# Kernel optimization log

Hardware: AMD Instinct MI355X
Metric: run time of the kernel (lower is better)

## Reference

```python
import jax, jax.numpy as jnp
import numpy as np

S, B, E, H = 2048, 2, 1024, 16
HD = E // H


def setup_inputs() -> dict:
    key = jax.random.key(0)
    ks = jax.random.split(key, 8)
    sc = 0.05
    return {
        "query": jax.random.normal(ks[0], (S, B, E), jnp.float32),
        "key": jax.random.normal(ks[1], (S, B, E), jnp.float32),
        "value": jax.random.normal(ks[2], (S, B, E), jnp.float32),
        "position_bias": jax.random.normal(ks[3], (B, S, S), jnp.float32) * sc,
        "in_proj_weight": jax.random.normal(ks[4], (3 * E, E), jnp.float32) * sc,
        "in_proj_bias": jnp.zeros((3 * E,), jnp.float32),
        "out_w": jax.random.normal(ks[5], (E, E), jnp.float32) * sc,
        "out_b": jnp.zeros((E,), jnp.float32),
    }


def reference(query, key, value, position_bias, in_proj_weight, in_proj_bias, out_w, out_b):
    # packed in-projection: w is (3E, E) in q,k,v order
    w_q, w_k, w_v = jnp.split(in_proj_weight, 3, axis=0)
    b_q, b_k, b_v = jnp.split(in_proj_bias, 3, axis=0)
    q = query @ w_q.T + b_q          # (S, B, E)
    k = key @ w_k.T + b_k
    v = value @ w_v.T + b_v
    # split heads: (S, B, H, HD)
    q = q.reshape(S, B, H, HD)
    k = k.reshape(S, B, H, HD)
    v = v.reshape(S, B, H, HD)
    scale = 1.0 / jnp.sqrt(jnp.float32(HD))
    # scores: (B, H, tgt, src)
    scores = jnp.einsum("qbhd,kbhd->bhqk", q * scale, k)
    scores = scores + position_bias[:, None, :, :]
    attn = jax.nn.softmax(scores, axis=-1)
    out = jnp.einsum("bhqk,kbhd->qbhd", attn, v).reshape(S, B, E)
    out = out @ out_w.T + out_b      # (S, B, E)
    attn_weights = attn.reshape(B * H, S, S)
    return out, attn_weights
```

## Files before the change

### kernel.cpp

```cpp
#include <hip/hip_runtime.h>

#define S_ 2048
#define B_ 2
#define E_ 1024
#define H_ 16

typedef _Float16 f16x8 __attribute__((ext_vector_type(8)));
typedef _Float16 f16x4 __attribute__((ext_vector_type(4)));
typedef _Float16 f16x2 __attribute__((ext_vector_type(2)));
typedef float f32x4 __attribute__((ext_vector_type(4)));
typedef unsigned short us4_t __attribute__((ext_vector_type(4)));
typedef unsigned u32x4 __attribute__((ext_vector_type(4)));
typedef unsigned u32x2 __attribute__((ext_vector_type(2)));

static __device__ __forceinline__ unsigned short f2h(float x) {
  _Float16 h = (_Float16)x;
  return __builtin_bit_cast(unsigned short, h);
}
static __device__ __forceinline__ unsigned pk_f16(float a, float b) {
  auto r = __builtin_amdgcn_cvt_pkrtz(a, b);
  return __builtin_bit_cast(unsigned, r);
}

__global__ void k_cvt_all(const float* __restrict__ q, const float* __restrict__ k,
                          const float* __restrict__ v, const float* __restrict__ ipw,
                          const float* __restrict__ outw, const float* __restrict__ posb,
                          unsigned short* __restrict__ qx, unsigned short* __restrict__ kx,
                          unsigned short* __restrict__ vx, unsigned short* __restrict__ w3,
                          unsigned short* __restrict__ ow, unsigned short* __restrict__ pb16) {
  const int M1 = 1 << 20;
  int i = blockIdx.x * blockDim.x + threadIdx.x;
  int stp = gridDim.x * blockDim.x;
  for (; i < 6 * M1; i += stp) {
    const float* src;
    unsigned short* dst;
    int j;
    if (i < M1)                   { src = q;    dst = qx;   j = i; }
    else if (i < 2 * M1)          { src = k;    dst = kx;   j = i - M1; }
    else if (i < 3 * M1)          { src = v;    dst = vx;   j = i - 2 * M1; }
    else if (i < 3 * M1 + 786432) { src = ipw;  dst = w3;   j = i - 3 * M1; }
    else if (i < 4 * M1)          { src = outw; dst = ow;   j = i - 3 * M1 - 786432; }
    else                          { src = posb; dst = pb16; j = i - 4 * M1; }
    f32x4 x = ((const f32x4*)src)[j];
    us4_t h;
    #pragma unroll
    for (int e = 0; e < 4; ++e) h[e] = f2h(x[e]);
    ((us4_t*)dst)[j] = h;
  }
}

__launch_bounds__(256, 2)
__global__ void k_proj_qk(const unsigned short* __restrict__ qx, const unsigned short* __restrict__ kx,
                          const unsigned short* __restrict__ wqk, const float* __restrict__ bias,
                          unsigned short* __restrict__ qf, unsigned short* __restrict__ kf) {
  const int z = blockIdx.z;
  const unsigned short* A = z ? kx : qx;
  const unsigned short* W = wqk + (size_t)z * (1024 * 1024);
  unsigned short* C = z ? kf : qf;
  const float* bia = bias + z * 1024;
  const float scale = z ? 1.0f : 0.125f;

  __shared__ unsigned short sA[128][40], sB[128][40];

  const int t = threadIdx.x;
  const int wid = t >> 6, l = t & 63, g = l >> 4, c = l & 15;
  const int wr = wid >> 1, wc = wid & 1;
  const int mb = blockIdx.x * 128, nb = blockIdx.y * 128;
  const int sr = t >> 1, sc = (t & 1) * 16;

  f32x4 acc[4][4] = {};

  for (int k0 = 0; k0 < 1024; k0 += 32) {
    __syncthreads();
    {
      const unsigned short* pa = A + (size_t)(mb + sr) * 1024 + k0 + sc;
      const unsigned short* pb = W + (size_t)(nb + sr) * 1024 + k0 + sc;
      *(f16x8*)&sA[sr][sc]     = *(const f16x8*)pa;
      *(f16x8*)&sA[sr][sc + 8] = *(const f16x8*)(pa + 8);
      *(f16x8*)&sB[sr][sc]     = *(const f16x8*)pb;
      *(f16x8*)&sB[sr][sc + 8] = *(const f16x8*)(pb + 8);
    }
    __syncthreads();
    f16x8 af[4], bf[4];
    #pragma unroll
    for (int i = 0; i < 4; ++i) {
      af[i] = *(const f16x8*)&sA[wr * 64 + i * 16 + c][g * 8];
      bf[i] = *(const f16x8*)&sB[wc * 64 + i * 16 + c][g * 8];
    }
    #pragma unroll
    for (int i = 0; i < 4; ++i)
      #pragma unroll
      for (int j = 0; j < 4; ++j)
        acc[i][j] = __builtin_amdgcn_mfma_f32_16x16x32_f16(af[i], bf[j], acc[i][j], 0, 0, 0);
  }
  #pragma unroll
  for (int i = 0; i < 4; ++i)
    #pragma unroll
    for (int j = 0; j < 4; ++j)
      #pragma unroll
      for (int rr = 0; rr < 4; ++rr) {
        int m = mb + wr * 64 + i * 16 + 4 * g + rr;
        int n = nb + wc * 64 + j * 16 + c;
        float v = (acc[i][j][rr] + bia[n]) * scale;
        C[(size_t)m * 1024 + n] = f2h(v);
      }
}

__launch_bounds__(256, 2)
__global__ void k_proj_v(const unsigned short* __restrict__ wv, const unsigned short* __restrict__ vx,
                         const float* __restrict__ bias, unsigned short* __restrict__ VT) {
  __shared__ unsigned short sA[128][40], sB[128][40];
  const int t = threadIdx.x;
  const int wid = t >> 6, l = t & 63, g = l >> 4, c = l & 15;
  const int wr = wid >> 1, wc = wid & 1;
  const int mb = blockIdx.x * 128;
  const int nb = blockIdx.y * 128;
  const int bb = nb >> 11;
  const int jb = nb & 2047;
  const int sr = t >> 1, sc = (t & 1) * 16;

  f32x4 acc[4][4] = {};
  for (int k0 = 0; k0 < 1024; k0 += 32) {
    __syncthreads();
    {
      const unsigned short* pa = wv + (size_t)(mb + sr) * 1024 + k0 + sc;
      const unsigned short* pb = vx + ((size_t)(jb + sr) * 2 + bb) * 1024 + k0 + sc;
      *(f16x8*)&sA[sr][sc]     = *(const f16x8*)pa;
      *(f16x8*)&sA[sr][sc + 8] = *(const f16x8*)(pa + 8);
      *(f16x8*)&sB[sr][sc]     = *(const f16x8*)pb;
      *(f16x8*)&sB[sr][sc + 8] = *(const f16x8*)(pb + 8);
    }
    __syncthreads();
    f16x8 af[4], bf[4];
    #pragma unroll
    for (int i = 0; i < 4; ++i) {
      af[i] = *(const f16x8*)&sA[wr * 64 + i * 16 + c][g * 8];
      bf[i] = *(const f16x8*)&sB[wc * 64 + i * 16 + c][g * 8];
    }
    #pragma unroll
    for (int i = 0; i < 4; ++i)
      #pragma unroll
      for (int j = 0; j < 4; ++j)
        acc[i][j] = __builtin_amdgcn_mfma_f32_16x16x32_f16(af[i], bf[j], acc[i][j], 0, 0, 0);
  }
  #pragma unroll
  for (int i = 0; i < 4; ++i)
    #pragma unroll
    for (int j = 0; j < 4; ++j)
      #pragma unroll
      for (int rr = 0; rr < 4; ++rr) {
        int m = mb + wr * 64 + i * 16 + 4 * g + rr;
        int jj = jb + wc * 64 + j * 16 + c;
        float v = acc[i][j][rr] + bias[2048 + m];
        VT[(size_t)bb * (1024 * 2048) + (size_t)m * 2048 + jj] = f2h(v);
      }
}

__launch_bounds__(256, 4)
__global__ void k_attn_pv(const unsigned short* __restrict__ qf, const unsigned short* __restrict__ kf,
                          const unsigned short* __restrict__ VT, const unsigned short* __restrict__ pb16,
                          float* __restrict__ attn, unsigned short* __restrict__ oc) {
  const int swz = (int)((blockIdx.x & 7) * 512 + (blockIdx.x >> 3));
  const int h = swz >> 8;
  const int b = (swz >> 7) & 1;
  const int qt = swz & 127;

  const int t = threadIdx.x;
  const int wid = t >> 6, l = t & 63, g = l >> 4, c = l & 15;
  const int ct = wid;

  __shared__ unsigned smem[8192];
  __shared__ float lds_red[4][16];
  unsigned* S_k = smem;
  unsigned* S_v = smem + 4096;

  const size_t qoff = ((size_t)(qt * 16 + c) * 2 + b) * 1024 + h * 64 + g * 8;
  const f16x8 qfr0 = *(const f16x8*)(qf + qoff);
  const f16x8 qfr1 = *(const f16x8*)(qf + qoff + 32);

  const unsigned short* kfb = kf + (size_t)b * 1024 + h * 64;
  const unsigned short* vtb = VT + ((size_t)b * 1024 + h * 64) * 2048;
  const unsigned short* pbRow = pb16 + (size_t)b * S_ * S_ + (size_t)(qt * 16 + c) * S_ + ct * 16;

  const int rb = t >> 3;
  const int lsl = (t & 7) ^ (rb & 7);

  #define LDSRD(base, row, slot) \
    __builtin_bit_cast(f16x8, *(const u32x4*)&(base)[(row) * 32 + ((((slot) ^ ((row) & 7))) * 4)])

  #define GLDS(stg, buf) do { \
    __builtin_amdgcn_global_load_lds( \
        (const __attribute__((address_space(1))) unsigned*)(kfb + (size_t)((stg) * 64 + rb) * 2048 + lsl * 8), \
        (__attribute__((address_space(3))) unsigned*)&S_k[(buf) * 2048 + wid * 256], 16, 0, 0); \
    __builtin_amdgcn_global_load_lds( \
        (const __attribute__((address_space(1))) unsigned*)(kfb + (size_t)((stg) * 64 + rb + 32) * 2048 + lsl * 8), \
        (__attribute__((address_space(3))) unsigned*)&S_k[(buf) * 2048 + 1024 + wid * 256], 16, 0, 0); \
    __builtin_amdgcn_global_load_lds( \
        (const __attribute__((address_space(1))) unsigned*)(vtb + (size_t)rb * 2048 + (stg) * 64 + lsl * 8), \
        (__attribute__((address_space(3))) unsigned*)&S_v[(buf) * 2048 + wid * 256], 16, 0, 0); \
    __builtin_amdgcn_global_load_lds( \
        (const __attribute__((address_space(1))) unsigned*)(vtb + (size_t)(rb + 32) * 2048 + (stg) * 64 + lsl * 8), \
        (__attribute__((address_space(3))) unsigned*)&S_v[(buf) * 2048 + 1024 + wid * 256], 16, 0, 0); \
  } while (0)

  f32x4 bias[2];
  unsigned psc0[32], psc1[32];
  float lsum = 0.f;
  f32x4 oacc[4] = {};

  GLDS(0, 0);
  {
    f16x4 b0 = *(const f16x4*)(pbRow + 4 * g);
    bias[0][0] = (float)b0[0] - 8.f; bias[0][1] = (float)b0[1] - 8.f;
    bias[0][2] = (float)b0[2] - 8.f; bias[0][3] = (float)b0[3] - 8.f;
  }
  __syncthreads();

  #pragma unroll
  for (int st = 0; st < 32; ++st) {
    const int cur = st & 1;
    if (st < 31) GLDS(st + 1, cur ^ 1);
    if (st < 31) {
      f16x4 bb = *(const f16x4*)(pbRow + (st + 1) * 64 + 4 * g);
      bias[cur ^ 1][0] = (float)bb[0] - 8.f; bias[cur ^ 1][1] = (float)bb[1] - 8.f;
      bias[cur ^ 1][2] = (float)bb[2] - 8.f; bias[cur ^ 1][3] = (float)bb[3] - 8.f;
    }

    {
      const int row = ct * 16 + c;
      const unsigned* kb = S_k + cur * 2048;
      f16x8 kfr0 = LDSRD(kb, row, g);
      f16x8 kfr1 = LDSRD(kb, row, 4 + g);
      f32x4 aA = {}, aB = {};
      aA = __builtin_amdgcn_mfma_f32_16x16x32_f16(kfr0, qfr0, aA, 0, 0, 0);
      aB = __builtin_amdgcn_mfma_f32_16x16x32_f16(kfr1, qfr1, aB, 0, 0, 0);
      float p0 = __expf(aA[0] + aB[0] + bias[cur][0]);
      float p1 = __expf(aA[1] + aB[1] + bias[cur][1]);
      float p2 = __expf(aA[2] + aB[2] + bias[cur][2]);
      float p3 = __expf(aA[3] + aB[3] + bias[cur][3]);
      lsum += (p0 + p1) + (p2 + p3);
      psc0[st] = pk_f16(p0, p1);
      psc1[st] = pk_f16(p2, p3);
    }

    {
      u32x2 br; br[0] = psc0[st]; br[1] = psc1[st];
      const f16x4 bfrag = __builtin_bit_cast(f16x4, br);
      const unsigned* vb = S_v + cur * 2048;
      #pragma unroll
      for (int dt = 0; dt < 4; ++dt) {
        const int row = dt * 16 + c;
        const int sl = (2 * ct + (g >> 1)) ^ (row & 7);
        u32x2 ar = *(const u32x2*)&vb[row * 32 + sl * 4 + 2 * (g & 1)];
        oacc[dt] = __builtin_amdgcn_mfma_f32_16x16x16f16(__builtin_bit_cast(f16x4, ar), bfrag, oacc[dt], 0, 0, 0);
      }
    }

    __syncthreads();
  }

  lsum += __shfl_xor(lsum, 16, 64);
  lsum += __shfl_xor(lsum, 32, 64);
  if (l < 16) lds_red[wid][l] = lsum;
  __syncthreads();
  const float inv = 1.0f / ((lds_red[0][c] + lds_red[1][c]) + (lds_red[2][c] + lds_red[3][c]));

  float* ored = (float*)smem;
  #pragma unroll
  for (int dt = 0; dt < 4; ++dt) {
    f32x4 o = oacc[dt];
    o[0] *= inv; o[1] *= inv; o[2] *= inv; o[3] *= inv;
    *(f32x4*)&ored[(wid * 16 + c) * 68 + dt * 16 + 4 * g] = o;
  }
  __syncthreads();
  {
    const int q = t >> 4;
    const int d0 = (t & 15) * 4;
    f32x4 s0 = *(const f32x4*)&ored[(0 * 16 + q) * 68 + d0];
    f32x4 s1 = *(const f32x4*)&ored[(1 * 16 + q) * 68 + d0];
    f32x4 s2 = *(const f32x4*)&ored[(2 * 16 + q) * 68 + d0];
    f32x4 s3 = *(const f32x4*)&ored[(3 * 16 + q) * 68 + d0];
    f32x4 s;
    s[0] = (s0[0] + s1[0]) + (s2[0] + s3[0]);
    s[1] = (s0[1] + s1[1]) + (s2[1] + s3[1]);
    s[2] = (s0[2] + s1[2]) + (s2[2] + s3[2]);
    s[3] = (s0[3] + s1[3]) + (s2[3] + s3[3]);
    u32x2 pk;
    pk[0] = pk_f16(s[0], s[1]);
    pk[1] = pk_f16(s[2], s[3]);
    *(u32x2*)&oc[((size_t)(qt * 16 + q) * 2 + b) * 1024 + h * 64 + d0] = pk;
  }

  float* arow = attn + ((size_t)(b * 16 + h) * S_ + qt * 16 + c) * S_ + ct * 16;
  #pragma unroll
  for (int st = 0; st < 32; ++st) {
    f16x2 h0 = __builtin_bit_cast(f16x2, psc0[st]);
    f16x2 h1 = __builtin_bit_cast(f16x2, psc1[st]);
    f32x4 o;
    o[0] = (float)h0[0] * inv;
    o[1] = (float)h0[1] * inv;
    o[2] = (float)h1[0] * inv;
    o[3] = (float)h1[1] * inv;
    *(f32x4*)(arow + (size_t)st * 64 + 4 * g) = o;
  }
  #undef LDSRD
  #undef GLDS
}

__launch_bounds__(256, 2)
__global__ void k_outproj(const unsigned short* __restrict__ oc, const unsigned short* __restrict__ ow,
                          const float* __restrict__ ob, float* __restrict__ out) {
  __shared__ unsigned short sA[128][40], sB[128][40];
  const int t = threadIdx.x;
  const int wid = t >> 6, l = t & 63, g = l >> 4, c = l & 15;
  const int wr = wid >> 1, wc = wid & 1;
  const int mb = blockIdx.x * 128, nb = blockIdx.y * 128;
  const int sr = t >> 1, sc = (t & 1) * 16;

  f32x4 acc[4][4] = {};
  for (int k0 = 0; k0 < 1024; k0 += 32) {
    __syncthreads();
    {
      const unsigned short* pa = oc + (size_t)(mb + sr) * 1024 + k0 + sc;
      const unsigned short* pb = ow + (size_t)(nb + sr) * 1024 + k0 + sc;
      *(f16x8*)&sA[sr][sc]     = *(const f16x8*)pa;
      *(f16x8*)&sA[sr][sc + 8] = *(const f16x8*)(pa + 8);
      *(f16x8*)&sB[sr][sc]     = *(const f16x8*)pb;
      *(f16x8*)&sB[sr][sc + 8] = *(const f16x8*)(pb + 8);
    }
    __syncthreads();
    f16x8 af[4], bf[4];
    #pragma unroll
    for (int i = 0; i < 4; ++i) {
      af[i] = *(const f16x8*)&sA[wr * 64 + i * 16 + c][g * 8];
      bf[i] = *(const f16x8*)&sB[wc * 64 + i * 16 + c][g * 8];
    }
    #pragma unroll
    for (int i = 0; i < 4; ++i)
      #pragma unroll
      for (int j = 0; j < 4; ++j)
        acc[i][j] = __builtin_amdgcn_mfma_f32_16x16x32_f16(af[i], bf[j], acc[i][j], 0, 0, 0);
  }
  #pragma unroll
  for (int i = 0; i < 4; ++i)
    #pragma unroll
    for (int j = 0; j < 4; ++j)
      #pragma unroll
      for (int rr = 0; rr < 4; ++rr) {
        int m = mb + wr * 64 + i * 16 + 4 * g + rr;
        int n = nb + wc * 64 + j * 16 + c;
        out[(size_t)m * 1024 + n] = acc[i][j][rr] + ob[n];
      }
}

extern "C" void kernel_launch(void* const* d_in, const int* in_sizes, int n_in,
                              void* d_out, int out_size, void* d_ws, size_t ws_size,
                              hipStream_t stream) {
  (void)in_sizes; (void)n_in; (void)out_size; (void)ws_size;
  const float* query = (const float*)d_in[0];
  const float* keyi  = (const float*)d_in[1];
  const float* value = (const float*)d_in[2];
  const float* posb  = (const float*)d_in[3];
  const float* ipw   = (const float*)d_in[4];
  const float* ipb   = (const float*)d_in[5];
  const float* outw  = (const float*)d_in[6];
  const float* outb  = (const float*)d_in[7];
  float* out = (float*)d_out;
  float* attn = out + (size_t)S_ * B_ * E_;

  char* ws = (char*)d_ws;
  size_t off = 0;
  auto alloc = [&](size_t bytes) -> void* {
    void* p = ws + off;
    off += (bytes + 255) & ~(size_t)255;
    return p;
  };
  const size_t NTOK = (size_t)S_ * B_;
  unsigned short* qx   = (unsigned short*)alloc(NTOK * 1024 * 2);
  unsigned short* kx   = (unsigned short*)alloc(NTOK * 1024 * 2);
  unsigned short* vx   = (unsigned short*)alloc(NTOK * 1024 * 2);
  unsigned short* w3   = (unsigned short*)alloc((size_t)3072 * 1024 * 2);
  unsigned short* ow   = (unsigned short*)alloc((size_t)1024 * 1024 * 2);
  unsigned short* pb16 = (unsigned short*)alloc((size_t)B_ * S_ * S_ * 2);
  unsigned short* qf   = (unsigned short*)alloc(NTOK * 1024 * 2);
  unsigned short* kf   = (unsigned short*)alloc(NTOK * 1024 * 2);
  unsigned short* VT   = (unsigned short*)alloc((size_t)2 * 1024 * 2048 * 2);
  unsigned short* oc   = (unsigned short*)alloc(NTOK * 1024 * 2);

  k_cvt_all<<<3072, 256, 0, stream>>>(query, keyi, value, ipw, outw, posb,
                                      qx, kx, vx, w3, ow, pb16);

  k_proj_qk<<<dim3(32, 8, 2), 256, 0, stream>>>(qx, kx, w3, ipb, qf, kf);
  k_proj_v<<<dim3(8, 32), 256, 0, stream>>>(w3 + (size_t)2048 * 1024, vx, ipb, VT);
  k_attn_pv<<<4096, 256, 0, stream>>>(qf, kf, VT, pb16, attn, oc);
  k_outproj<<<dim3(32, 8), 256, 0, stream>>>(oc, ow, outb, out);
}
```

Baseline: 355.2 us.

## Process two query tiles per attention block to share K/V LDS staging

The attention kernel now uses 512-thread blocks that each cover 32 query rows (two 16-row tiles), with 8 waves split into query-tile × column-tile groups. Each K/V stage loaded into LDS now serves twice as many queries, which halves the global K/V traffic and the staging work per query, and the grid shrinks to 2048 blocks. In exchange, larger blocks with more barrier participants may lower occupancy flexibility, and the extra syncthreads plus the enlarged shared array add overhead.

```diff
diff --git a/kernel.cpp b/kernel.cpp
--- a/kernel.cpp
+++ b/kernel.cpp
@@ -156,31 +156,32 @@
       }
 }
 
-__launch_bounds__(256, 4)
+__launch_bounds__(512, 2)
 __global__ void k_attn_pv(const unsigned short* __restrict__ qf, const unsigned short* __restrict__ kf,
                           const unsigned short* __restrict__ VT, const unsigned short* __restrict__ pb16,
                           float* __restrict__ attn, unsigned short* __restrict__ oc) {
-  const int swz = (int)((blockIdx.x & 7) * 512 + (blockIdx.x >> 3));
-  const int h = swz >> 8;
-  const int b = (swz >> 7) & 1;
-  const int qt = swz & 127;
+  const int swz = (int)((blockIdx.x & 7) * 256 + (blockIdx.x >> 3));
+  const int h = swz >> 7;
+  const int b = (swz >> 6) & 1;
+  const int qt2 = swz & 63;
 
   const int t = threadIdx.x;
   const int wid = t >> 6, l = t & 63, g = l >> 4, c = l & 15;
-  const int ct = wid;
-
-  __shared__ unsigned smem[8192];
-  __shared__ float lds_red[4][16];
+  const int qtile = wid >> 2, ctile = wid & 3;
+
+  __shared__ unsigned smem[8704];
+  __shared__ float lds_red[8][16];
   unsigned* S_k = smem;
   unsigned* S_v = smem + 4096;
 
-  const size_t qoff = ((size_t)(qt * 16 + c) * 2 + b) * 1024 + h * 64 + g * 8;
+  const int qrow = qt2 * 32 + qtile * 16 + c;
+  const size_t qoff = ((size_t)qrow * 2 + b) * 1024 + h * 64 + g * 8;
   const f16x8 qfr0 = *(const f16x8*)(qf + qoff);
   const f16x8 qfr1 = *(const f16x8*)(qf + qoff + 32);
 
   const unsigned short* kfb = kf + (size_t)b * 1024 + h * 64;
   const unsigned short* vtb = VT + ((size_t)b * 1024 + h * 64) * 2048;
-  const unsigned short* pbRow = pb16 + (size_t)b * S_ * S_ + (size_t)(qt * 16 + c) * S_ + ct * 16;
+  const unsigned short* pbRow = pb16 + (size_t)b * S_ * S_ + (size_t)qrow * S_ + ctile * 16;
 
   const int rb = t >> 3;
   const int lsl = (t & 7) ^ (rb & 7);
@@ -193,14 +194,8 @@
         (const __attribute__((address_space(1))) unsigned*)(kfb + (size_t)((stg) * 64 + rb) * 2048 + lsl * 8), \
         (__attribute__((address_space(3))) unsigned*)&S_k[(buf) * 2048 + wid * 256], 16, 0, 0); \
     __builtin_amdgcn_global_load_lds( \
-        (const __attribute__((address_space(1))) unsigned*)(kfb + (size_t)((stg) * 64 + rb + 32) * 2048 + lsl * 8), \
-        (__attribute__((address_space(3))) unsigned*)&S_k[(buf) * 2048 + 1024 + wid * 256], 16, 0, 0); \
-    __builtin_amdgcn_global_load_lds( \
         (const __attribute__((address_space(1))) unsigned*)(vtb + (size_t)rb * 2048 + (stg) * 64 + lsl * 8), \
         (__attribute__((address_space(3))) unsigned*)&S_v[(buf) * 2048 + wid * 256], 16, 0, 0); \
-    __builtin_amdgcn_global_load_lds( \
-        (const __attribute__((address_space(1))) unsigned*)(vtb + (size_t)(rb + 32) * 2048 + (stg) * 64 + lsl * 8), \
-        (__attribute__((address_space(3))) unsigned*)&S_v[(buf) * 2048 + 1024 + wid * 256], 16, 0, 0); \
   } while (0)
 
   f32x4 bias[2];
@@ -227,7 +222,7 @@
     }
 
     {
-      const int row = ct * 16 + c;
+      const int row = ctile * 16 + c;
       const unsigned* kb = S_k + cur * 2048;
       f16x8 kfr0 = LDSRD(kb, row, g);
       f16x8 kfr1 = LDSRD(kb, row, 4 + g);
@@ -250,7 +245,7 @@
       #pragma unroll
       for (int dt = 0; dt < 4; ++dt) {
         const int row = dt * 16 + c;
-        const int sl = (2 * ct + (g >> 1)) ^ (row & 7);
+        const int sl = (2 * ctile + (g >> 1)) ^ (row & 7);
         u32x2 ar = *(const u32x2*)&vb[row * 32 + sl * 4 + 2 * (g & 1)];
         oacc[dt] = __builtin_amdgcn_mfma_f32_16x16x16f16(__builtin_bit_cast(f16x4, ar), bfrag, oacc[dt], 0, 0, 0);
       }
@@ -263,9 +258,12 @@
   lsum += __shfl_xor(lsum, 32, 64);
   if (l < 16) lds_red[wid][l] = lsum;
   __syncthreads();
-  const float inv = 1.0f / ((lds_red[0][c] + lds_red[1][c]) + (lds_red[2][c] + lds_red[3][c]));
+  const int gb = qtile * 4;
+  const float inv = 1.0f / ((lds_red[gb + 0][c] + lds_red[gb + 1][c]) +
+                            (lds_red[gb + 2][c] + lds_red[gb + 3][c]));
 
   float* ored = (float*)smem;
+  __syncthreads();
   #pragma unroll
   for (int dt = 0; dt < 4; ++dt) {
     f32x4 o = oacc[dt];
@@ -274,12 +272,15 @@
   }
   __syncthreads();
   {
-    const int q = t >> 4;
-    const int d0 = (t & 15) * 4;
-    f32x4 s0 = *(const f32x4*)&ored[(0 * 16 + q) * 68 + d0];
-    f32x4 s1 = *(const f32x4*)&ored[(1 * 16 + q) * 68 + d0];
-    f32x4 s2 = *(const f32x4*)&ored[(2 * 16 + q) * 68 + d0];
-    f32x4 s3 = *(const f32x4*)&ored[(3 * 16 + q) * 68 + d0];
+    const int q_i = t >> 8;
+    const int rem = t & 255;
+    const int q = rem >> 4;
+    const int d0 = (rem & 15) * 4;
+    const int wb = q_i * 4;
+    f32x4 s0 = *(const f32x4*)&ored[((wb + 0) * 16 + q) * 68 + d0];
+    f32x4 s1 = *(const f32x4*)&ored[((wb + 1) * 16 + q) * 68 + d0];
+    f32x4 s2 = *(const f32x4*)&ored[((wb + 2) * 16 + q) * 68 + d0];
+    f32x4 s3 = *(const f32x4*)&ored[((wb + 3) * 16 + q) * 68 + d0];
     f32x4 s;
     s[0] = (s0[0] + s1[0]) + (s2[0] + s3[0]);
     s[1] = (s0[1] + s1[1]) + (s2[1] + s3[1]);
@@ -288,10 +289,10 @@
     u32x2 pk;
     pk[0] = pk_f16(s[0], s[1]);
     pk[1] = pk_f16(s[2], s[3]);
-    *(u32x2*)&oc[((size_t)(qt * 16 + q) * 2 + b) * 1024 + h * 64 + d0] = pk;
-  }
-
-  float* arow = attn + ((size_t)(b * 16 + h) * S_ + qt * 16 + c) * S_ + ct * 16;
+    *(u32x2*)&oc[((size_t)(qt2 * 32 + q_i * 16 + q) * 2 + b) * 1024 + h * 64 + d0] = pk;
+  }
+
+  float* arow = attn + ((size_t)(b * 16 + h) * S_ + qrow) * S_ + ctile * 16;
   #pragma unroll
   for (int st = 0; st < 32; ++st) {
     f16x2 h0 = __builtin_bit_cast(f16x2, psc0[st]);
@@ -392,6 +393,6 @@
 
   k_proj_qk<<<dim3(32, 8, 2), 256, 0, stream>>>(qx, kx, w3, ipb, qf, kf);
   k_proj_v<<<dim3(8, 32), 256, 0, stream>>>(w3 + (size_t)2048 * 1024, vx, ipb, VT);
-  k_attn_pv<<<4096, 256, 0, stream>>>(qf, kf, VT, pb16, attn, oc);
+  k_attn_pv<<<2048, 512, 0, stream>>>(qf, kf, VT, pb16, attn, oc);
   k_outproj<<<dim3(32, 8), 256, 0, stream>>>(oc, ow, outb, out);
 }
```

Measured after the change: 452.9 us. +27.5%, slower.
